# Kernel optimization log

Measured on AMD Instinct MI355X. Metric: run time of the kernel, lower is better.

Reference implementation:

```python
import jax, jax.numpy as jnp
import numpy as np

B, S, HID = 8, 1024, 1024
NH, HD = 16, 64  # num heads, head dim; NH*HD == HID


def setup_inputs() -> dict:
    key = jax.random.key(0)
    ks = jax.random.split(key, 8)
    sc = 0.02
    return {
        "hidden_states": jax.random.normal(ks[0], (B, S, HID), jnp.float32),
        "attention_mask": jnp.zeros((B, 1, 1, S), jnp.float32),
        "Wq": jax.random.normal(ks[1], (HID, HID), jnp.float32) * sc,
        "bq": jnp.zeros((HID,), jnp.float32),
        "Wk": jax.random.normal(ks[2], (HID, HID), jnp.float32) * sc,
        "bk": jnp.zeros((HID,), jnp.float32),
        "Wv": jax.random.normal(ks[3], (HID, HID), jnp.float32) * sc,
        "bv": jnp.zeros((HID,), jnp.float32),
    }


def reference(hidden_states, attention_mask, Wq, bq, Wk, bk, Wv, bv):
    def split_heads(x):  # [B,S,HID] -> [B,NH,S,HD]
        return x.reshape(B, S, NH, HD).transpose(0, 2, 1, 3)

    q = split_heads(hidden_states @ Wq + bq)
    k = split_heads(hidden_states @ Wk + bk)
    v = split_heads(hidden_states @ Wv + bv)

    # [B,NH,S,S] score matrix, scale, additive mask, softmax
    scores = jnp.einsum("bhqd,bhkd->bhqk", q, k) / jnp.sqrt(jnp.float32(HD))
    scores = scores + attention_mask
    probs = jax.nn.softmax(scores, axis=-1)  # dropout prob = 0.0 -> identity

    ctx = jnp.einsum("bhqk,bhkd->bhqd", probs, v)
    return ctx.transpose(0, 2, 1, 3).reshape(B, S, HID)
```

## Files before the change

### kernel.cpp

```cpp
#include <hip/hip_runtime.h>


typedef __bf16 bf16x8 __attribute__((ext_vector_type(8)));
typedef float f32x16 __attribute__((ext_vector_type(16)));

__device__ __forceinline__ unsigned rne16(float x) {
  unsigned u = __builtin_bit_cast(unsigned, x);
  return (u + 0x7fffu + ((u >> 16) & 1u)) >> 16;
}
__device__ __forceinline__ unsigned packbf(float lo, float hi) {
  return rne16(lo) | (rne16(hi) << 16);
}
__device__ __forceinline__ unsigned packbf_fast(float lo, float hi) {
  unsigned ul = __builtin_bit_cast(unsigned, lo) + 0x8000u;
  unsigned uh = __builtin_bit_cast(unsigned, hi) + 0x8000u;
  return __builtin_amdgcn_perm(uh, ul, 0x07060302u);
}
__device__ __forceinline__ void async16(void* l, const void* g) {
  __builtin_amdgcn_global_load_lds((const __attribute__((address_space(1))) void*)g,
                                   (__attribute__((address_space(3))) void*)l, 16, 0, 0);
}

__global__ __launch_bounds__(256) void k_prep(const float* __restrict__ h,
                                              unsigned short* __restrict__ hbf,
                                              const float* __restrict__ Wq,
                                              const float* __restrict__ Wk,
                                              const float* __restrict__ Wv,
                                              unsigned short* __restrict__ wt) {
  __shared__ float t[32][33];
  int bid = blockIdx.x, tid = threadIdx.x;
  if (bid < 8192) {
    size_t i = (size_t)bid * 256 + tid;
    float4 v = ((const float4*)h)[i];
    uint2 r;
    r.x = packbf(v.x, v.y);
    r.y = packbf(v.z, v.w);
    ((uint2*)hbf)[i] = r;
  } else {
    int id = bid - 8192;
    int which = id >> 10;
    int sub = id & 1023;
    int c0 = (sub & 31) * 32, k0 = (sub >> 5) * 32;
    const float* W = which == 0 ? Wq : (which == 1 ? Wk : Wv);
    int tx = tid & 31, ty = tid >> 5;
#pragma unroll
    for (int i = 0; i < 4; ++i) {
      int r = ty + i * 8;
      t[r][tx] = W[(size_t)(k0 + r) * 1024 + c0 + tx];
    }
    __syncthreads();
#pragma unroll
    for (int i = 0; i < 4; ++i) {
      int r = ty + i * 8;
      wt[((size_t)which * 1024 + c0 + r) * 1024 + k0 + tx] = (unsigned short)rne16(t[tx][r]);
    }
  }
}

__global__ __launch_bounds__(256, 2) void k_gemm(const unsigned short* __restrict__ A,
                                                 const unsigned short* __restrict__ Bm,
                                                 const float* __restrict__ bq,
                                                 const float* __restrict__ bk,
                                                 const float* __restrict__ bv,
                                                 unsigned short* __restrict__ qkv,
                                                 unsigned short* __restrict__ vt) {
  __shared__ __align__(16) char lds[49152];
  int tid = threadIdx.x, w = tid >> 6, lane = tid & 63, l5 = lane & 31, q5 = lane >> 5;
  int wr = w >> 1, wc = w & 1;
  int m0 = blockIdx.x * 256, n0 = blockIdx.y * 128;

  f32x16 acc[4][2];
#pragma unroll
  for (int i = 0; i < 4; ++i)
#pragma unroll
    for (int j = 0; j < 2; ++j)
#pragma unroll
      for (int e = 0; e < 16; ++e) acc[i][j][e] = 0.f;

  auto stage = [&](int kt, char* buf) {
    int k0 = kt * 32;
#pragma unroll
    for (int t = 0; t < 6; ++t) {
      int idx = w * 6 + t;
      if (idx < 16) {
        int mt = idx >> 1, ks = idx & 1;
        async16(buf + idx * 1024,
                A + (size_t)(m0 + mt * 32 + l5) * 1024 + k0 + ks * 16 + q5 * 8);
      } else {
        int i2 = idx - 16, nt = i2 >> 1, ks = i2 & 1;
        async16(buf + 16384 + i2 * 1024,
                Bm + (size_t)(n0 + nt * 32 + l5) * 1024 + k0 + ks * 16 + q5 * 8);
      }
    }
  };

  auto compute = [&](const char* buf) {
#pragma unroll
    for (int ks = 0; ks < 2; ++ks) {
      bf16x8 b0 = *(const bf16x8*)(buf + 16384 + ((wc * 2 + 0) * 2 + ks) * 1024 + lane * 16);
      bf16x8 b1 = *(const bf16x8*)(buf + 16384 + ((wc * 2 + 1) * 2 + ks) * 1024 + lane * 16);
#pragma unroll
      for (int mt = 0; mt < 4; ++mt) {
        bf16x8 a = *(const bf16x8*)(buf + ((wr * 4 + mt) * 2 + ks) * 1024 + lane * 16);
        acc[mt][0] = __builtin_amdgcn_mfma_f32_32x32x16_bf16(a, b0, acc[mt][0], 0, 0, 0);
        acc[mt][1] = __builtin_amdgcn_mfma_f32_32x32x16_bf16(a, b1, acc[mt][1], 0, 0, 0);
      }
    }
  };

  char* buf0 = lds;
  char* buf1 = lds + 24576;
  stage(0, buf0);
#pragma unroll 1
  for (int kt = 0; kt < 32; kt += 2) {
    __syncthreads();
    if (kt + 1 < 32) stage(kt + 1, buf1);
    compute(buf0);
    __syncthreads();
    if (kt + 2 < 32) stage(kt + 2, buf0);
    compute(buf1);
  }

  int which = n0 >> 10;
  if (which != 2) {
    const float* bp = which == 0 ? bq : bk;
    unsigned short* dst = qkv + (size_t)which * 8388608;
#pragma unroll
    for (int nt = 0; nt < 2; ++nt) {
      int n_in = (n0 & 1023) + wc * 64 + nt * 32 + l5;
      float bias = bp[n_in];
      int hh = n_in >> 6, d = n_in & 63;
#pragma unroll
      for (int mt = 0; mt < 4; ++mt) {
#pragma unroll
        for (int e = 0; e < 16; ++e) {
          int m = m0 + wr * 128 + mt * 32 + (e & 3) + 8 * (e >> 2) + 4 * q5;
          int b = m >> 10, s = m & 1023;
          dst[((size_t)(b * 16 + hh) << 16) + (s << 6) + d] =
              (unsigned short)rne16(acc[mt][nt][e] + bias);
        }
      }
    }
  } else {
    int b = m0 >> 10;
    unsigned short* scr = (unsigned short*)(lds) + w * 2176;
#pragma unroll
    for (int mt = 0; mt < 4; ++mt) {
#pragma unroll
      for (int nt = 0; nt < 2; ++nt) {
        int n_in = (n0 & 1023) + wc * 64 + nt * 32 + l5;
        float bias = bv[n_in];
        unsigned short* tile = scr + nt * 1088;
#pragma unroll
        for (int jj = 0; jj < 8; ++jj) {
          int e = 2 * jj;
          int s_loc = (e & 3) + 8 * (e >> 2) + 4 * q5;
          *(unsigned*)(tile + l5 * 34 + s_loc) =
              packbf(acc[mt][nt][e] + bias, acc[mt][nt][e + 1] + bias);
        }
      }
#pragma unroll
      for (int nt = 0; nt < 2; ++nt) {
        const unsigned short* tile = scr + nt * 1088;
        unsigned di[8];
#pragma unroll
        for (int i = 0; i < 8; ++i)
          di[i] = *(const unsigned*)(tile + l5 * 34 + q5 * 16 + i * 2);
        int n_in = (n0 & 1023) + wc * 64 + nt * 32 + l5;
        int hh = n_in >> 6, dd = n_in & 63;
        int s_base = (m0 & 1023) + wr * 128 + mt * 32 + q5 * 16;
        unsigned short* dst = vt + ((size_t)(b * 16 + hh) * 64 + dd) * 1024 + s_base;
        uint4 v0 = {di[0], di[1], di[2], di[3]};
        uint4 v1 = {di[4], di[5], di[6], di[7]};
        *(uint4*)(dst) = v0;
        *(uint4*)(dst + 8) = v1;
      }
    }
  }
}

__global__ __launch_bounds__(256, 4) void k_attn(const unsigned short* __restrict__ qg,
                                                 const unsigned short* __restrict__ kg,
                                                 const unsigned short* __restrict__ vtg,
                                                 const float* __restrict__ maskg,
                                                 float* __restrict__ out) {
  __shared__ __align__(16) char lds[36864];
  char* KF = lds;
  char* VF = lds + 16384;
  float* MK = (float*)(lds + 32768);
  int tid = threadIdx.x, w = tid >> 6, lane = tid & 63, l5 = lane & 31, q5 = lane >> 5;
  int idx = blockIdx.x;
  int bi = idx & 7;
  int j = idx >> 3;
  int h = j >> 3, qc = j & 7;
  int bh = bi * 16 + h, s0 = qc * 128;
  const unsigned short* qb = qg + ((size_t)bh << 16);
  const unsigned short* kb = kg + ((size_t)bh << 16);
  const unsigned short* vb = vtg + ((size_t)bh << 16);
  const float LG = 1.4426950408889634f;
  const float C1 = 0.125f * LG;

  {
    float4 mv = *(const float4*)(maskg + (size_t)bi * 1024 + tid * 4);
    mv.x *= LG; mv.y *= LG; mv.z *= LG; mv.w *= LG;
    *(float4*)(MK + tid * 4) = mv;
  }

  bf16x8 qfr[4];
#pragma unroll
  for (int ds = 0; ds < 4; ++ds)
    qfr[ds] = *(const bf16x8*)(qb + (size_t)(s0 + w * 32 + l5) * 64 + ds * 16 + q5 * 8);

  f32x16 O[2];
#pragma unroll
  for (int i = 0; i < 2; ++i)
#pragma unroll
    for (int e = 0; e < 16; ++e) O[i][e] = 0.f;
  float lsum = 0.f;

#pragma unroll 1
  for (int kt = 0; kt < 8; ++kt) {
    int k0 = kt * 128;
    __syncthreads();
#pragma unroll
    for (int t = 0; t < 4; ++t) {
      int f = w * 4 + t, mt = f >> 2, ds = f & 3;
      async16(KF + f * 1024, kb + (size_t)(k0 + mt * 32 + l5) * 64 + ds * 16 + q5 * 8);
    }
#pragma unroll
    for (int t = 0; t < 4; ++t) {
      int f = w * 4 + t, dt = f >> 3, ks = f & 7;
      async16(VF + f * 1024, vb + (size_t)(dt * 32 + l5) * 1024 + k0 + ks * 16 + q5 * 8);
    }
    __syncthreads();

#pragma unroll
    for (int mt = 0; mt < 4; ++mt) {
      f32x16 S;
#pragma unroll
      for (int e = 0; e < 16; ++e) S[e] = 0.f;
#pragma unroll
      for (int ds = 0; ds < 4; ++ds) {
        bf16x8 a = *(const bf16x8*)(KF + (mt * 4 + ds) * 1024 + lane * 16);
        S = __builtin_amdgcn_mfma_f32_32x32x16_bf16(a, qfr[ds], S, 0, 0, 0);
      }
      float p[16];
#pragma unroll
      for (int g4 = 0; g4 < 4; ++g4) {
        float4 mv = *(const float4*)(MK + k0 + mt * 32 + g4 * 8 + q5 * 4);
        p[g4 * 4 + 0] = __builtin_amdgcn_exp2f(S[g4 * 4 + 0] * C1 + mv.x);
        p[g4 * 4 + 1] = __builtin_amdgcn_exp2f(S[g4 * 4 + 1] * C1 + mv.y);
        p[g4 * 4 + 2] = __builtin_amdgcn_exp2f(S[g4 * 4 + 2] * C1 + mv.z);
        p[g4 * 4 + 3] = __builtin_amdgcn_exp2f(S[g4 * 4 + 3] * C1 + mv.w);
      }
      unsigned p2[8];
#pragma unroll
      for (int e = 0; e < 16; ++e) lsum += p[e];
#pragma unroll
      for (int jj = 0; jj < 8; ++jj) p2[jj] = packbf_fast(p[2 * jj], p[2 * jj + 1]);
#pragma unroll
      for (int kh = 0; kh < 2; ++kh) {
        int ks = mt * 2 + kh, gp = kh * 4;
        bf16x8 av0 = *(const bf16x8*)(VF + (0 * 8 + ks) * 1024 + lane * 16);
        bf16x8 av1 = *(const bf16x8*)(VF + (1 * 8 + ks) * 1024 + lane * 16);
        unsigned o0 = p2[gp + 0], o1 = p2[gp + 1];
        unsigned o2 = p2[gp + 2], o3 = p2[gp + 3];
        unsigned t0 = __shfl_xor((int)o0, 32);
        unsigned t1 = __shfl_xor((int)o1, 32);
        unsigned t2 = __shfl_xor((int)o2, 32);
        unsigned t3 = __shfl_xor((int)o3, 32);
        uint4 fu;
        fu.x = q5 ? t2 : o0;
        fu.y = q5 ? t3 : o1;
        fu.z = q5 ? o2 : t0;
        fu.w = q5 ? o3 : t1;
        bf16x8 bfrag = __builtin_bit_cast(bf16x8, fu);
        O[0] = __builtin_amdgcn_mfma_f32_32x32x16_bf16(av0, bfrag, O[0], 0, 0, 0);
        O[1] = __builtin_amdgcn_mfma_f32_32x32x16_bf16(av1, bfrag, O[1], 0, 0, 0);
      }
    }
  }

  __syncthreads();
  float* Ob = (float*)(lds + w * 8192);
  float lt = lsum + __shfl_xor(lsum, 32);
  float rinv = 1.0f / lt;
#pragma unroll
  for (int dt = 0; dt < 2; ++dt)
#pragma unroll
    for (int g4 = 0; g4 < 4; ++g4) {
      float4 val;
      val.x = O[dt][g4 * 4 + 0] * rinv;
      val.y = O[dt][g4 * 4 + 1] * rinv;
      val.z = O[dt][g4 * 4 + 2] * rinv;
      val.w = O[dt][g4 * 4 + 3] * rinv;
      int c = dt * 8 + g4 * 2 + q5;
      *(float4*)(Ob + l5 * 64 + (c ^ (l5 & 15)) * 4) = val;
    }
#pragma unroll
  for (int t = 0; t < 8; ++t) {
    int qr = t * 4 + (lane >> 4), cr = lane & 15;
    float4 vv = *(const float4*)(Ob + qr * 64 + (cr ^ (qr & 15)) * 4);
    int s = s0 + w * 32 + qr;
    *(float4*)(out + (((size_t)(bi * 1024 + s)) << 10) + (h << 6) + (cr << 2)) = vv;
  }
}

extern "C" void kernel_launch(void* const* d_in, const int* in_sizes, int n_in,
                              void* d_out, int out_size, void* d_ws, size_t ws_size,
                              hipStream_t stream) {
  (void)in_sizes; (void)n_in; (void)out_size; (void)ws_size;
  const float* hidden = (const float*)d_in[0];
  const float* mask = (const float*)d_in[1];
  const float* Wq = (const float*)d_in[2];
  const float* bq = (const float*)d_in[3];
  const float* Wk = (const float*)d_in[4];
  const float* bk = (const float*)d_in[5];
  const float* Wv = (const float*)d_in[6];
  const float* bv = (const float*)d_in[7];
  float* out = (float*)d_out;
  char* ws = (char*)d_ws;
  unsigned short* hbf = (unsigned short*)ws;
  unsigned short* wt  = (unsigned short*)(ws + 16777216);
  unsigned short* qkv = (unsigned short*)(ws + 23068672);
  unsigned short* vt  = (unsigned short*)(ws + 56623104);

  k_prep<<<11264, 256, 0, stream>>>(hidden, hbf, Wq, Wk, Wv, wt);
  k_gemm<<<dim3(32, 24), 256, 0, stream>>>(hbf, wt, bq, bk, bv, qkv, vt);
  k_attn<<<1024, 256, 0, stream>>>(qkv, qkv + 8388608, vt, mask, out);
}
```

Measured before the change: 254.5 us.

## Double-buffer K/V tiles in attention kernel with 512-thread blocks over 256 queries

The attention kernel now runs 8 waves per block, each block covering 256 query rows instead of 128. Each block therefore loads every K/V tile once for twice as many queries, halving global K/V traffic. K/V tiles are staged with async global-to-LDS loads into two alternating 32 KB buffers, so the next tile's load overlaps the current tile's MFMA and softmax work. The cost is higher LDS use per block (about 68 KB) and half as many blocks, which may lower occupancy and latency hiding.

```diff
diff --git a/kernel.cpp b/kernel.cpp
--- a/kernel.cpp
+++ b/kernel.cpp
@@ -179,21 +179,21 @@
   }
 }
 
-__global__ __launch_bounds__(256, 4) void k_attn(const unsigned short* __restrict__ qg,
+__global__ __launch_bounds__(512, 4) void k_attn(const unsigned short* __restrict__ qg,
                                                  const unsigned short* __restrict__ kg,
                                                  const unsigned short* __restrict__ vtg,
                                                  const float* __restrict__ maskg,
                                                  float* __restrict__ out) {
-  __shared__ __align__(16) char lds[36864];
-  char* KF = lds;
-  char* VF = lds + 16384;
-  float* MK = (float*)(lds + 32768);
+  __shared__ __align__(16) char lds[69632];
+  char* B0 = lds;
+  char* B1 = lds + 32768;
+  float* MK = (float*)(lds + 65536);
   int tid = threadIdx.x, w = tid >> 6, lane = tid & 63, l5 = lane & 31, q5 = lane >> 5;
   int idx = blockIdx.x;
   int bi = idx & 7;
   int j = idx >> 3;
-  int h = j >> 3, qc = j & 7;
-  int bh = bi * 16 + h, s0 = qc * 128;
+  int h = j & 15, qc = j >> 4;
+  int bh = bi * 16 + h, s0 = qc * 256;
   const unsigned short* qb = qg + ((size_t)bh << 16);
   const unsigned short* kb = kg + ((size_t)bh << 16);
   const unsigned short* vb = vtg + ((size_t)bh << 16);
@@ -201,9 +201,10 @@
   const float C1 = 0.125f * LG;
 
   {
-    float4 mv = *(const float4*)(maskg + (size_t)bi * 1024 + tid * 4);
-    mv.x *= LG; mv.y *= LG; mv.z *= LG; mv.w *= LG;
-    *(float4*)(MK + tid * 4) = mv;
+    float2 mv = *(const float2*)(maskg + (size_t)bi * 1024 + tid * 2);
+    mv.x *= LG;
+    mv.y *= LG;
+    *(float2*)(MK + tid * 2) = mv;
   }
 
   bf16x8 qfr[4];
@@ -218,22 +219,26 @@
     for (int e = 0; e < 16; ++e) O[i][e] = 0.f;
   float lsum = 0.f;
 
-#pragma unroll 1
-  for (int kt = 0; kt < 8; ++kt) {
+  auto stage = [&](int kt, char* buf) {
     int k0 = kt * 128;
-    __syncthreads();
 #pragma unroll
     for (int t = 0; t < 4; ++t) {
-      int f = w * 4 + t, mt = f >> 2, ds = f & 3;
-      async16(KF + f * 1024, kb + (size_t)(k0 + mt * 32 + l5) * 64 + ds * 16 + q5 * 8);
-    }
-#pragma unroll
-    for (int t = 0; t < 4; ++t) {
-      int f = w * 4 + t, dt = f >> 3, ks = f & 7;
-      async16(VF + f * 1024, vb + (size_t)(dt * 32 + l5) * 1024 + k0 + ks * 16 + q5 * 8);
-    }
-    __syncthreads();
-
+      int f = w * 4 + t;
+      if (f < 16) {
+        int mt = f >> 2, ds = f & 3;
+        async16(buf + f * 1024, kb + (size_t)(k0 + mt * 32 + l5) * 64 + ds * 16 + q5 * 8);
+      } else {
+        int f2 = f - 16, dt = f2 >> 3, ks = f2 & 7;
+        async16(buf + 16384 + f2 * 1024,
+                vb + (size_t)(dt * 32 + l5) * 1024 + k0 + ks * 16 + q5 * 8);
+      }
+    }
+  };
+
+  auto compute = [&](int kt, const char* buf) {
+    const char* KF = buf;
+    const char* VF = buf + 16384;
+    int k0 = kt * 128;
 #pragma unroll
     for (int mt = 0; mt < 4; ++mt) {
       f32x16 S;
@@ -279,6 +284,17 @@
         O[1] = __builtin_amdgcn_mfma_f32_32x32x16_bf16(av1, bfrag, O[1], 0, 0, 0);
       }
     }
+  };
+
+  stage(0, B0);
+#pragma unroll 1
+  for (int kt = 0; kt < 8; kt += 2) {
+    __syncthreads();
+    if (kt + 1 < 8) stage(kt + 1, B1);
+    compute(kt, B0);
+    __syncthreads();
+    if (kt + 2 < 8) stage(kt + 2, B0);
+    compute(kt + 1, B1);
   }
 
   __syncthreads();
@@ -327,5 +343,5 @@
 
   k_prep<<<11264, 256, 0, stream>>>(hidden, hbf, Wq, Wk, Wv, wt);
   k_gemm<<<dim3(32, 24), 256, 0, stream>>>(hbf, wt, bq, bk, bv, qkv, vt);
-  k_attn<<<1024, 256, 0, stream>>>(qkv, qkv + 8388608, vt, mask, out);
-}
+  k_attn<<<512, 512, 0, stream>>>(qkv, qkv + 8388608, vt, mask, out);
+}
```

Result: slower. 288.1 us (+13.2%).
